# Kernel optimization log

Measured on AMD Instinct MI355X. Metric: run time of the kernel, lower is better.

The kernel has to match this reference:

```python
import jax, jax.numpy as jnp
import numpy as np

EPS = 0.001

def _conv1x1(h, w, b):
    # h: [n,c,v,w_dim], w: [o,c], b: [o]  -> [n,o,v,w_dim]
    return jnp.einsum('ncvw,oc->novw', h, w) + b[None, :, None, None]

def setup_inputs() -> dict:
    key = jax.random.key(0)
    ks = jax.random.split(key, 10)
    N, Cin, T, V = 16, 64, 64, 384
    inp = {
        'x': jax.random.normal(ks[0], (N, Cin, T, V), dtype=jnp.float32),
        'A': jax.random.uniform(ks[1], (N, 8, V, V), dtype=jnp.float32),
        'conv_w': jax.random.normal(ks[2], (64, Cin), dtype=jnp.float32) * 0.05,
        'conv_b': jax.random.normal(ks[3], (64,), dtype=jnp.float32) * 0.05,
        'w1': jax.random.normal(ks[4], (16, 7), dtype=jnp.float32) * 0.2,
        'b1': jax.random.normal(ks[5], (16,), dtype=jnp.float32) * 0.05,
        'w2': jax.random.normal(ks[6], (32, 16), dtype=jnp.float32) * 0.2,
        'b2': jax.random.normal(ks[7], (32,), dtype=jnp.float32) * 0.05,
        'w3': jax.random.normal(ks[8], (64, 32), dtype=jnp.float32) * 0.2,
        'b3': jax.random.normal(ks[9], (64,), dtype=jnp.float32) * 0.05,
    }
    return inp

def reference(x, A, conv_w, conv_b, w1, b1, w2, b2, w3, b3):
    # self.conv: 1x1 conv (t_kernel_size=1) mapping in_channels -> out_channels*kernel_size = 64
    x = jnp.einsum('nctv,oc->notv', x, conv_w) + conv_b[None, :, None, None]
    mask = A[:, 7][:, None]              # [n,1,v,w]
    h = A[:, :7]                         # [n,7,v,w]
    # adjmatder: three 1x1 convs with ReLU (dropout = identity in eval mode)
    h = jax.nn.relu(_conv1x1(h, w1, b1))
    h = jax.nn.relu(_conv1x1(h, w2, b2))
    h = jax.nn.relu(_conv1x1(h, w3, b3))   # [n,64,v,w]
    Am = h * mask
    Dl = 1.0 / (Am.sum(axis=2) + EPS)      # degree-inverse over v: [n,64,w]
    An = Am * Dl[:, :, None, :]            # einsum 'ncvw,ncw->ncvw'
    out = jnp.einsum('nctv,ncvw->nctw', x, An)
    return out, An
```

## Files before the change

kernel.cpp:

```cpp
#include <hip/hip_runtime.h>

#define EPS_F 0.001f

constexpr int Nn = 16;
constexpr int Cc = 64;
constexpr int Tt = 64;
constexpr int Vv = 384;
constexpr size_t TV = (size_t)Tt * Vv;
constexpr size_t VW = (size_t)Vv * Vv;
constexpr size_t OUT0 = (size_t)Nn * Cc * TV;

__global__ __launch_bounds__(256) void k_conv(const float* __restrict__ x,
        const float* __restrict__ cw, const float* __restrict__ cb,
        float* __restrict__ xc) {
    __shared__ float wt[64 * 64];
    const int tid = threadIdx.x;
    for (int i = tid; i < 4096; i += 256) {
        int o = i & 63, c = i >> 6;
        wt[c * 64 + o] = cw[o * 64 + c];
    }
    __syncthreads();
    const int b = blockIdx.x;
    const int n = b / 48;
    const int pos = (b % 48) * 512 + tid;
    const float* xin = x + (size_t)n * Cc * TV + pos;
    float acc0[64], acc1[64];
#pragma unroll
    for (int o = 0; o < 64; ++o) { acc0[o] = 0.f; acc1[o] = 0.f; }
    for (int c = 0; c < 64; ++c) {
        float x0 = xin[(size_t)c * TV];
        float x1 = xin[(size_t)c * TV + 256];
        const float4* wr = (const float4*)(wt + c * 64);
#pragma unroll
        for (int oq = 0; oq < 16; ++oq) {
            float4 w4 = wr[oq];
            acc0[oq*4+0] += x0 * w4.x; acc0[oq*4+1] += x0 * w4.y;
            acc0[oq*4+2] += x0 * w4.z; acc0[oq*4+3] += x0 * w4.w;
            acc1[oq*4+0] += x1 * w4.x; acc1[oq*4+1] += x1 * w4.y;
            acc1[oq*4+2] += x1 * w4.z; acc1[oq*4+3] += x1 * w4.w;
        }
    }
    float* xo = xc + (size_t)n * Cc * TV + pos;
#pragma unroll
    for (int o = 0; o < 64; ++o) {
        float bo = cb[o];
        xo[(size_t)o * TV]       = acc0[o] + bo;
        xo[(size_t)o * TV + 256] = acc1[o] + bo;
    }
}

__device__ __forceinline__ void mlp12(const float a[8],
        const float* __restrict__ w1, const float* __restrict__ b1,
        const float* __restrict__ w2, const float* __restrict__ b2,
        float h2[32]) {
    float h1[16];
#pragma unroll
    for (int o = 0; o < 16; ++o) {
        float t = b1[o];
#pragma unroll
        for (int k = 0; k < 7; ++k) t += w1[o * 7 + k] * a[k];
        h1[o] = fmaxf(t, 0.f);
    }
#pragma unroll
    for (int o = 0; o < 32; ++o) {
        float t = b2[o];
#pragma unroll
        for (int i = 0; i < 16; ++i) t += w2[o * 16 + i] * h1[i];
        h2[o] = fmaxf(t, 0.f);
    }
}

__global__ __launch_bounds__(384) void k_am(const float* __restrict__ A,
        const float* __restrict__ w1, const float* __restrict__ b1,
        const float* __restrict__ w2, const float* __restrict__ b2,
        const float* __restrict__ w3, const float* __restrict__ b3,
        float* __restrict__ Am) {
    const int tid = threadIdx.x;
    const int b = blockIdx.x;
    const int n = b / 384;
    const int v = b % 384;
    const float* Ab = A + (size_t)n * 8 * VW + (size_t)v * Vv + tid;
    float a[8];
#pragma unroll
    for (int k = 0; k < 8; ++k) a[k] = Ab[(size_t)k * VW];
    float h2[32];
    mlp12(a, w1, b1, w2, b2, h2);
    const float mask = a[7];
    float* ap = Am + (size_t)n * 64 * VW + (size_t)v * Vv + tid;
#pragma unroll
    for (int o = 0; o < 64; ++o) {
        float t = b3[o];
#pragma unroll
        for (int i = 0; i < 32; ++i) t += w3[o * 32 + i] * h2[i];
        ap[(size_t)o * VW] = fmaxf(t, 0.f) * mask;
    }
}

__global__ __launch_bounds__(256) void k_gemm(const float* __restrict__ xc,
        float* __restrict__ An, float* __restrict__ out) {
    __shared__ float As[16 * 68];
    __shared__ float Bs[16 * 68];
    __shared__ float4 part[256];
    __shared__ __align__(16) float dlr[64];
    const int tid = threadIdx.x;
    const int b = blockIdx.x;
    const int batch = b / 6;
    const int w0 = (b % 6) * 64;
    const float* Ap = xc + (size_t)batch * TV;
    float* Bp = An + (size_t)batch * VW + w0;
    const int ty = tid / 16, tx = tid % 16;
    const int lr = tid / 4,  lq = tid % 4;
    const int br = tid / 16, bc = tid % 16;
    float acc[4][4];
#pragma unroll
    for (int i = 0; i < 4; ++i)
#pragma unroll
        for (int j = 0; j < 4; ++j) acc[i][j] = 0.f;
    float4 cs = make_float4(0.f, 0.f, 0.f, 0.f);
    for (int k0 = 0; k0 < 384; k0 += 16) {
        float4 a4 = *(const float4*)(Ap + (size_t)lr * 384 + k0 + lq * 4);
        float4 b4 = *(const float4*)(Bp + (size_t)(k0 + br) * 384 + bc * 4);
        cs.x += b4.x; cs.y += b4.y; cs.z += b4.z; cs.w += b4.w;
        As[(lq*4+0)*68 + lr] = a4.x;
        As[(lq*4+1)*68 + lr] = a4.y;
        As[(lq*4+2)*68 + lr] = a4.z;
        As[(lq*4+3)*68 + lr] = a4.w;
        *(float4*)(Bs + br * 68 + bc * 4) = b4;
        __syncthreads();
#pragma unroll
        for (int kk = 0; kk < 16; ++kk) {
            float4 av = *(const float4*)(As + kk * 68 + ty * 4);
            float4 bv = *(const float4*)(Bs + kk * 68 + tx * 4);
            float aa[4] = {av.x, av.y, av.z, av.w};
            float bb[4] = {bv.x, bv.y, bv.z, bv.w};
#pragma unroll
            for (int i = 0; i < 4; ++i)
#pragma unroll
                for (int j = 0; j < 4; ++j) acc[i][j] += aa[i] * bb[j];
        }
        __syncthreads();
    }
    part[tid] = cs;
    __syncthreads();
    if (tid < 64) {
        const int q = tid >> 2, e = tid & 3;
        float s = 0.f;
#pragma unroll
        for (int r = 0; r < 16; ++r) {
            const float* p4 = (const float*)&part[r * 16 + q];
            s += p4[e];
        }
        dlr[tid] = 1.f / (s + EPS_F);
    }
    __syncthreads();
    const float4 d4 = *(const float4*)(dlr + tx * 4);
    for (int k0 = 0; k0 < 384; k0 += 16) {
        float* bp = Bp + (size_t)(k0 + br) * 384 + bc * 4;
        float4 v = *(const float4*)bp;
        v.x *= d4.x; v.y *= d4.y; v.z *= d4.z; v.w *= d4.w;
        *(float4*)bp = v;
    }
    float* op = out + (size_t)batch * TV + w0 + tx * 4;
#pragma unroll
    for (int i = 0; i < 4; ++i) {
        float4 o4 = make_float4(acc[i][0] * d4.x, acc[i][1] * d4.y,
                                acc[i][2] * d4.z, acc[i][3] * d4.w);
        *(float4*)(op + (size_t)(ty * 4 + i) * 384) = o4;
    }
}

extern "C" void kernel_launch(void* const* d_in, const int* in_sizes, int n_in,
                              void* d_out, int out_size, void* d_ws, size_t ws_size,
                              hipStream_t stream) {
    const float* x  = (const float*)d_in[0];
    const float* A  = (const float*)d_in[1];
    const float* cw = (const float*)d_in[2];
    const float* cb = (const float*)d_in[3];
    const float* w1 = (const float*)d_in[4];
    const float* b1 = (const float*)d_in[5];
    const float* w2 = (const float*)d_in[6];
    const float* b2 = (const float*)d_in[7];
    const float* w3 = (const float*)d_in[8];
    const float* b3 = (const float*)d_in[9];

    float* out = (float*)d_out;
    float* An  = out + OUT0;
    float* xc  = (float*)d_ws;

    k_conv<<<768, 256, 0, stream>>>(x, cw, cb, xc);
    k_am  <<<6144, 384, 0, stream>>>(A, w1, b1, w2, b2, w3, b3, An);
    k_gemm<<<6144, 256, 0, stream>>>(xc, An, out);
}
```

Baseline: 1.431 ms.

## Stage MLP weights in LDS, process two rows per block, prefetch GEMM tiles

k_am now copies the MLP weights and biases into shared memory and has each block handle two v rows, so weights are reused across two outputs and half as many blocks are launched. k_gemm gains register prefetching of the next A and B tiles, so global loads overlap with the inner FMA loop. k_gemm also remaps block indices so that consecutive blocks are spread across batches/channels, aiming for better spread of memory traffic across the device. These changes raise register pressure in k_am, which holds two sets of activations, and add a shared-memory staging step at the start of every block.

```diff
diff --git a/kernel.cpp b/kernel.cpp
--- a/kernel.cpp
+++ b/kernel.cpp
@@ -49,50 +49,78 @@
     }
 }
 
-__device__ __forceinline__ void mlp12(const float a[8],
-        const float* __restrict__ w1, const float* __restrict__ b1,
-        const float* __restrict__ w2, const float* __restrict__ b2,
-        float h2[32]) {
-    float h1[16];
-#pragma unroll
-    for (int o = 0; o < 16; ++o) {
-        float t = b1[o];
-#pragma unroll
-        for (int k = 0; k < 7; ++k) t += w1[o * 7 + k] * a[k];
-        h1[o] = fmaxf(t, 0.f);
-    }
-#pragma unroll
-    for (int o = 0; o < 32; ++o) {
-        float t = b2[o];
-#pragma unroll
-        for (int i = 0; i < 16; ++i) t += w2[o * 16 + i] * h1[i];
-        h2[o] = fmaxf(t, 0.f);
-    }
-}
-
 __global__ __launch_bounds__(384) void k_am(const float* __restrict__ A,
         const float* __restrict__ w1, const float* __restrict__ b1,
         const float* __restrict__ w2, const float* __restrict__ b2,
         const float* __restrict__ w3, const float* __restrict__ b3,
         float* __restrict__ Am) {
+    __shared__ __align__(16) float sw1[16 * 8];
+    __shared__ __align__(16) float sw2[32 * 16];
+    __shared__ __align__(16) float sw3[64 * 32];
+    __shared__ float sb1[16], sb2[32], sb3[64];
     const int tid = threadIdx.x;
+    if (tid < 128) {
+        int o = tid >> 3, k = tid & 7;
+        sw1[tid] = (k < 7) ? w1[o * 7 + k] : 0.f;
+    }
+    for (int i = tid; i < 512; i += 384)  sw2[i] = w2[i];
+    for (int i = tid; i < 2048; i += 384) sw3[i] = w3[i];
+    if (tid < 16) sb1[tid] = b1[tid];
+    else if (tid < 48) sb2[tid - 16] = b2[tid - 16];
+    else if (tid < 112) sb3[tid - 48] = b3[tid - 48];
+    __syncthreads();
+
     const int b = blockIdx.x;
-    const int n = b / 384;
-    const int v = b % 384;
-    const float* Ab = A + (size_t)n * 8 * VW + (size_t)v * Vv + tid;
-    float a[8];
-#pragma unroll
-    for (int k = 0; k < 8; ++k) a[k] = Ab[(size_t)k * VW];
-    float h2[32];
-    mlp12(a, w1, b1, w2, b2, h2);
-    const float mask = a[7];
-    float* ap = Am + (size_t)n * 64 * VW + (size_t)v * Vv + tid;
+    const int n = b / 192;
+    const int v0 = (b % 192) * 2;
+    const float* Ab = A + (size_t)n * 8 * VW + (size_t)v0 * Vv + tid;
+    float aA[8], aB[8];
+#pragma unroll
+    for (int k = 0; k < 8; ++k) {
+        aA[k] = Ab[(size_t)k * VW];
+        aB[k] = Ab[(size_t)k * VW + Vv];
+    }
+    float h1A[16], h1B[16];
+#pragma unroll
+    for (int o = 0; o < 16; ++o) {
+        float4 wa = *(const float4*)(sw1 + o * 8);
+        float4 wb = *(const float4*)(sw1 + o * 8 + 4);
+        float tA = sb1[o], tB = sb1[o];
+        tA += wa.x*aA[0] + wa.y*aA[1] + wa.z*aA[2] + wa.w*aA[3];
+        tA += wb.x*aA[4] + wb.y*aA[5] + wb.z*aA[6] + wb.w*aA[7];
+        tB += wa.x*aB[0] + wa.y*aB[1] + wa.z*aB[2] + wa.w*aB[3];
+        tB += wb.x*aB[4] + wb.y*aB[5] + wb.z*aB[6] + wb.w*aB[7];
+        h1A[o] = fmaxf(tA, 0.f);
+        h1B[o] = fmaxf(tB, 0.f);
+    }
+    float h2A[32], h2B[32];
+#pragma unroll
+    for (int o = 0; o < 32; ++o) {
+        const float4* wr = (const float4*)(sw2 + o * 16);
+        float tA = sb2[o], tB = sb2[o];
+#pragma unroll
+        for (int q = 0; q < 4; ++q) {
+            float4 w4 = wr[q];
+            tA += w4.x*h1A[q*4+0] + w4.y*h1A[q*4+1] + w4.z*h1A[q*4+2] + w4.w*h1A[q*4+3];
+            tB += w4.x*h1B[q*4+0] + w4.y*h1B[q*4+1] + w4.z*h1B[q*4+2] + w4.w*h1B[q*4+3];
+        }
+        h2A[o] = fmaxf(tA, 0.f);
+        h2B[o] = fmaxf(tB, 0.f);
+    }
+    const float mA = aA[7], mB = aB[7];
+    float* apA = Am + (size_t)n * 64 * VW + (size_t)v0 * Vv + tid;
 #pragma unroll
     for (int o = 0; o < 64; ++o) {
-        float t = b3[o];
-#pragma unroll
-        for (int i = 0; i < 32; ++i) t += w3[o * 32 + i] * h2[i];
-        ap[(size_t)o * VW] = fmaxf(t, 0.f) * mask;
+        const float4* wr = (const float4*)(sw3 + o * 32);
+        float tA = sb3[o], tB = sb3[o];
+#pragma unroll
+        for (int q = 0; q < 8; ++q) {
+            float4 w4 = wr[q];
+            tA += w4.x*h2A[q*4+0] + w4.y*h2A[q*4+1] + w4.z*h2A[q*4+2] + w4.w*h2A[q*4+3];
+            tB += w4.x*h2B[q*4+0] + w4.y*h2B[q*4+1] + w4.z*h2B[q*4+2] + w4.w*h2B[q*4+3];
+        }
+        apA[(size_t)o * VW]      = fmaxf(tA, 0.f) * mA;
+        apA[(size_t)o * VW + Vv] = fmaxf(tB, 0.f) * mB;
     }
 }
 
@@ -103,7 +131,8 @@
     __shared__ float4 part[256];
     __shared__ __align__(16) float dlr[64];
     const int tid = threadIdx.x;
-    const int b = blockIdx.x;
+    const int bid = blockIdx.x;
+    const int b = (bid & 7) * 768 + (bid >> 3);
     const int batch = b / 6;
     const int w0 = (b % 6) * 64;
     const float* Ap = xc + (size_t)batch * TV;
@@ -117,9 +146,9 @@
 #pragma unroll
         for (int j = 0; j < 4; ++j) acc[i][j] = 0.f;
     float4 cs = make_float4(0.f, 0.f, 0.f, 0.f);
+    float4 a4 = *(const float4*)(Ap + (size_t)lr * 384 + lq * 4);
+    float4 b4 = *(const float4*)(Bp + (size_t)br * 384 + bc * 4);
     for (int k0 = 0; k0 < 384; k0 += 16) {
-        float4 a4 = *(const float4*)(Ap + (size_t)lr * 384 + k0 + lq * 4);
-        float4 b4 = *(const float4*)(Bp + (size_t)(k0 + br) * 384 + bc * 4);
         cs.x += b4.x; cs.y += b4.y; cs.z += b4.z; cs.w += b4.w;
         As[(lq*4+0)*68 + lr] = a4.x;
         As[(lq*4+1)*68 + lr] = a4.y;
@@ -127,6 +156,10 @@
         As[(lq*4+3)*68 + lr] = a4.w;
         *(float4*)(Bs + br * 68 + bc * 4) = b4;
         __syncthreads();
+        if (k0 + 16 < 384) {
+            a4 = *(const float4*)(Ap + (size_t)lr * 384 + (k0 + 16) + lq * 4);
+            b4 = *(const float4*)(Bp + (size_t)(k0 + 16 + br) * 384 + bc * 4);
+        }
 #pragma unroll
         for (int kk = 0; kk < 16; ++kk) {
             float4 av = *(const float4*)(As + kk * 68 + ty * 4);
@@ -188,6 +221,6 @@
     float* xc  = (float*)d_ws;
 
     k_conv<<<768, 256, 0, stream>>>(x, cw, cb, xc);
-    k_am  <<<6144, 384, 0, stream>>>(A, w1, b1, w2, b2, w3, b3, An);
+    k_am  <<<3072, 384, 0, stream>>>(A, w1, b1, w2, b2, w3, b3, An);
     k_gemm<<<6144, 256, 0, stream>>>(xc, An, out);
 }
```

After: 1.404 ms. Within noise of the previous version (-1.9%).
